# Kernel tuning notes

Hardware: AMD Instinct MI355X
Metric: run time of the kernel (lower is better)

The kernel has to match this reference:

```python
import jax, jax.numpy as jnp
import numpy as np

B, T = 64, 2048
D, H, L, OUT, V = 128, 256, 2, 64, 1000


def lstm_layer(x, Wih, Whh, bih, bhh):
    """Single-direction LSTM layer, PyTorch gate order (i, f, g, o).
    x: [B, T, Din] -> [B, T, H]"""
    Bn = x.shape[0]
    Hh = Whh.shape[1]
    # precompute input contribution to gates once: [B, T, 4H] -> time-major
    xg = jnp.einsum('btd,gd->btg', x, Wih) + bih
    xg = jnp.swapaxes(xg, 0, 1)  # [T, B, 4H]

    def step(carry, g_x):
        h, c = carry
        g = g_x + h @ Whh.T + bhh
        i, f, gg, o = jnp.split(g, 4, axis=-1)
        c = jax.nn.sigmoid(f) * c + jax.nn.sigmoid(i) * jnp.tanh(gg)
        h = jax.nn.sigmoid(o) * jnp.tanh(c)
        return (h, c), h

    h0 = jnp.zeros((Bn, Hh), x.dtype)
    (_, _), hs = jax.lax.scan(step, (h0, h0), xg)
    return jnp.swapaxes(hs, 0, 1)  # [B, T, H]


def setup_inputs() -> dict:
    key = jax.random.key(0)
    ks = jax.random.split(key, 12)
    s = 0.05
    inp = {
        'x': jax.random.randint(ks[0], (B, T), 0, V + 1, dtype=jnp.int32),
        'embed_table': jax.random.normal(ks[1], (V + 1, D), jnp.float32) * s,
        'W_ih0': jax.random.normal(ks[2], (4 * H, D), jnp.float32) * s,
        'W_hh0': jax.random.normal(ks[3], (4 * H, H), jnp.float32) * s,
        'b_ih0': jax.random.normal(ks[4], (4 * H,), jnp.float32) * s,
        'b_hh0': jax.random.normal(ks[5], (4 * H,), jnp.float32) * s,
        'W_ih1': jax.random.normal(ks[6], (4 * H, H), jnp.float32) * s,
        'W_hh1': jax.random.normal(ks[7], (4 * H, H), jnp.float32) * s,
        'b_ih1': jax.random.normal(ks[8], (4 * H,), jnp.float32) * s,
        'b_hh1': jax.random.normal(ks[9], (4 * H,), jnp.float32) * s,
        'fc_W': jax.random.normal(ks[10], (OUT, H), jnp.float32) * s,
        'fc_b': jax.random.normal(ks[11], (OUT,), jnp.float32) * s,
    }
    return inp


def reference(x, embed_table, W_ih0, W_hh0, b_ih0, b_hh0,
              W_ih1, W_hh1, b_ih1, b_hh1, fc_W, fc_b):
    # embedding + padding mask (padding_idx=0, masked_fill x==0 -> 0)
    e = embed_table[x]                              # [B, T, D]
    e = e * (x != 0)[..., None].astype(e.dtype)
    # 2-layer LSTM, zero initial state
    h = lstm_layer(e, W_ih0, W_hh0, b_ih0, b_hh0)   # [B, T, H]
    h = lstm_layer(h, W_ih1, W_hh1, b_ih1, b_hh1)   # [B, T, H]
    # linear + softmax over last dim
    logits = jnp.einsum('bth,oh->bto', h, fc_W) + fc_b
    return jax.nn.softmax(logits, axis=-1)
```

## Files before the change

kernel.cpp:

```cpp
#include <hip/hip_runtime.h>
#include <cstdint>
#include <cstddef>


typedef _Float16 half_t;
typedef _Float16 half8 __attribute__((ext_vector_type(8)));
typedef _Float16 half2t __attribute__((ext_vector_type(2)));
typedef float floatx4 __attribute__((ext_vector_type(4)));

#define B_   64
#define T_   2048
#define D_   128
#define H_   256
#define G4_  1024
#define OUT_ 64
#define MTOT (B_ * T_)

#define EVC  25
#define TLC  7
#define TL_BYTES (TLC * 1024 * 16)

#if defined(__has_builtin)
#if __has_builtin(__builtin_amdgcn_fdot2)
#define HAVE_FDOT2 1
#endif
#endif

__device__ __forceinline__ float dot2acc(unsigned w, unsigned h, float acc) {
  half2t a = __builtin_bit_cast(half2t, w);
  half2t b = __builtin_bit_cast(half2t, h);
#ifdef HAVE_FDOT2
  return __builtin_amdgcn_fdot2(a, b, acc, false);
#else
  return acc + (float)a[0] * (float)b[0] + (float)a[1] * (float)b[1];
#endif
}

__device__ __forceinline__ float fast_sigmoid(float x) {
  return 1.f / (1.f + __expf(-x));
}
__device__ __forceinline__ float fast_tanh(float x) {
  return 1.f - 2.f / (1.f + __expf(2.f * x));
}


__global__ __launch_bounds__(256) void k_cvt_f16(const float* __restrict__ in,
                                                 half_t* __restrict__ out, int n) {
  int i = blockIdx.x * 256 + threadIdx.x;
  if (i < n) out[i] = (half_t)in[i];
}

__global__ __launch_bounds__(256) void k_pack_whh(const float* __restrict__ whh,
                                                  half_t* __restrict__ wp) {
  int i = blockIdx.x * 256 + threadIdx.x;
  int e  = i & 7;
  int j  = (i >> 3) & 1023;
  int kc = i >> 13;
  wp[i] = (half_t)whh[j * 256 + kc * 8 + e];
}

__global__ __launch_bounds__(256) void k_bias(const float* __restrict__ a,
                                              const float* __restrict__ b,
                                              float* __restrict__ out, int n) {
  int i = blockIdx.x * 256 + threadIdx.x;
  if (i < n) out[i] = a[i] + b[i];
}

__global__ __launch_bounds__(256) void k_fcwt(const float* __restrict__ fcw,
                                              float* __restrict__ fcwt) {
  int i = blockIdx.x * 256 + threadIdx.x;
  fcwt[i] = fcw[(i & 63) * 256 + (i >> 6)];
}


__global__ __launch_bounds__(256) void k_embed(const int* __restrict__ x,
                                               const float* __restrict__ tab,
                                               half_t* __restrict__ e) {
  const long i = (long)blockIdx.x * 256 + threadIdx.x;
  const long m = i >> 4;
  const int ch = (int)(i & 15) * 8;
  const int xi = x[m];
  half8 v;
  #pragma unroll
  for (int q = 0; q < 8; ++q) v[q] = (half_t)0.f;
  if (xi != 0) {
    const float* p = tab + (long)xi * D_ + ch;
    #pragma unroll
    for (int q = 0; q < 8; ++q) v[q] = (half_t)p[q];
  }
  *(half8*)(e + m * D_ + ch) = v;
}


__global__ __launch_bounds__(256) void k_gemm_f16(const half_t* __restrict__ A,
                                                  const half_t* __restrict__ Wt,
                                                  const float* __restrict__ bias,
                                                  half_t* __restrict__ C,
                                                  int K, int N,
                                                  int rowShift, int strideB, int toff) {
  __shared__ half_t As[128][40];
  __shared__ half_t Bs[128][40];
  const int tid  = threadIdx.x;
  const int lane = tid & 63;
  const int wave = tid >> 6;
  const int wr = wave >> 1, wc = wave & 1;
  const int r0 = blockIdx.x * 128;
  const int n0 = blockIdx.y * 128;
  const int srow = tid >> 2;
  const int schunk = (tid & 3) * 8;
  const int rmask = (1 << rowShift) - 1;

  floatx4 zero = {0.f, 0.f, 0.f, 0.f};
  floatx4 acc[4][4];
  for (int i = 0; i < 4; ++i)
    for (int j = 0; j < 4; ++j) acc[i][j] = zero;

  const int ra = r0 + srow, rb = r0 + srow + 64;
  const half_t* ArowA = A + ((long)(ra >> rowShift) * strideB + toff + (ra & rmask)) * K;
  const half_t* ArowB = A + ((long)(rb >> rowShift) * strideB + toff + (rb & rmask)) * K;

  for (int k0 = 0; k0 < K; k0 += 32) {
    *(uint4*)(&As[srow][schunk])      = *(const uint4*)(ArowA + k0 + schunk);
    *(uint4*)(&As[srow + 64][schunk]) = *(const uint4*)(ArowB + k0 + schunk);
    const half_t* Bp = Wt + (long)(n0 + srow) * K + k0 + schunk;
    *(uint4*)(&Bs[srow][schunk])      = *(const uint4*)(Bp);
    *(uint4*)(&Bs[srow + 64][schunk]) = *(const uint4*)(Bp + 64L * K);
    __syncthreads();

    const int kq = (lane >> 4) * 8;
    const int fr = lane & 15;
    half8 af[4], bf[4];
    #pragma unroll
    for (int i = 0; i < 4; ++i) af[i] = *(const half8*)(&As[wr * 64 + i * 16 + fr][kq]);
    #pragma unroll
    for (int i = 0; i < 4; ++i) bf[i] = *(const half8*)(&Bs[wc * 64 + i * 16 + fr][kq]);
    #pragma unroll
    for (int mi = 0; mi < 4; ++mi)
      #pragma unroll
      for (int ni = 0; ni < 4; ++ni)
        acc[mi][ni] = __builtin_amdgcn_mfma_f32_16x16x32_f16(af[mi], bf[ni], acc[mi][ni], 0, 0, 0);
    __syncthreads();
  }

  const int fr = lane & 15, fq = lane >> 4;
  for (int ni = 0; ni < 4; ++ni) {
    const int gcol = n0 + wc * 64 + ni * 16 + fr;
    const float bv = bias[gcol];
    for (int mi = 0; mi < 4; ++mi) {
      const long grow = r0 + wr * 64 + mi * 16 + fq * 4;
      #pragma unroll
      for (int r = 0; r < 4; ++r)
        C[(grow + r) * (long)N + gcol] = (half_t)(acc[mi][ni][r] + bv);
    }
  }
}


__global__ __launch_bounds__(1024) void k_lstm_res(const half_t* __restrict__ xg,
                                                   const uint4* __restrict__ Wp,
                                                   half_t* __restrict__ hout,
                                                   float* __restrict__ c_state,
                                                   half_t* __restrict__ h_state,
                                                   int steps, int first) {
  extern __shared__ uint4 wtail[];
  __shared__ float gsh[1024];
  __shared__ __align__(16) half_t hsh[256];
  const int b = blockIdx.x;
  const int j = threadIdx.x;

  uint4 wv[EVC];
  #pragma unroll
  for (int kc = 0; kc < EVC; ++kc) wv[kc] = Wp[kc * 1024 + j];
  #pragma unroll
  for (int cc = 0; cc < TLC; ++cc) wtail[cc * 1024 + j] = Wp[(EVC + cc) * 1024 + j];

  float c = 0.f;
  if (j < H_) {
    if (first) {
      hsh[j] = (half_t)0.f;
    } else {
      hsh[j] = h_state[b * H_ + j];
      c = c_state[b * H_ + j];
    }
  }

  const half_t* xp = xg + (long)b * steps * G4_ + j;
  half_t* hp_out = hout + (long)b * steps * H_;
  half_t xv = xp[0];

  for (int t = 0; t < steps; ++t) {
    const int tn = (t + 1 < steps) ? t + 1 : t;
    half_t xnext = xp[(long)tn * G4_];
    __syncthreads();
    float acc = (float)xv;
    const uint4* hv4 = (const uint4*)hsh;
    #pragma unroll
    for (int kc = 0; kc < EVC; ++kc) {
      uint4 w = wv[kc];
      uint4 h4 = hv4[kc];
      acc = dot2acc(w.x, h4.x, acc);
      acc = dot2acc(w.y, h4.y, acc);
      acc = dot2acc(w.z, h4.z, acc);
      acc = dot2acc(w.w, h4.w, acc);
    }
    #pragma unroll
    for (int cc = 0; cc < TLC; ++cc) {
      uint4 w = wtail[cc * 1024 + j];
      uint4 h4 = hv4[EVC + cc];
      acc = dot2acc(w.x, h4.x, acc);
      acc = dot2acc(w.y, h4.y, acc);
      acc = dot2acc(w.z, h4.z, acc);
      acc = dot2acc(w.w, h4.w, acc);
    }
    gsh[j] = acc;
    xv = xnext;
    __syncthreads();
    if (j < H_) {
      float ig = fast_sigmoid(gsh[j]);
      float fg = fast_sigmoid(gsh[H_ + j]);
      float g2 = fast_tanh(gsh[2 * H_ + j]);
      float og = fast_sigmoid(gsh[3 * H_ + j]);
      c = fg * c + ig * g2;
      float h = og * fast_tanh(c);
      half_t hh = (half_t)h;
      hp_out[(long)t * H_ + j] = hh;
      hsh[j] = hh;
    }
  }
  if (j < H_) {
    c_state[b * H_ + j] = c;
    h_state[b * H_ + j] = hsh[j];
  }
}


__global__ __launch_bounds__(1024) void k_lstm(const half_t* __restrict__ xg,
                                               const uint4* __restrict__ Wp,
                                               half_t* __restrict__ hout,
                                               float* __restrict__ c_state,
                                               half_t* __restrict__ h_state,
                                               int steps, int first) {
  const int b = blockIdx.x;
  const int j = threadIdx.x;
  __shared__ float gsh[1024];
  __shared__ __align__(16) half_t hsh[256];
  float c = 0.f;
  if (j < H_) {
    if (first) {
      hsh[j] = (half_t)0.f;
    } else {
      hsh[j] = h_state[b * H_ + j];
      c = c_state[b * H_ + j];
    }
  }
  const uint4*  wp     = Wp + j;
  const half_t* xp     = xg + (long)b * steps * G4_ + j;
  half_t*       hp_out = hout + (long)b * steps * H_;
  for (int t = 0; t < steps; ++t) {
    __syncthreads();
    float acc = (float)xp[(long)t * G4_];
    const uint4* hv4 = (const uint4*)hsh;
    #pragma unroll 8
    for (int kc = 0; kc < 32; ++kc) {
      uint4 w  = wp[(long)kc * G4_];
      uint4 h4 = hv4[kc];
      acc = dot2acc(w.x, h4.x, acc);
      acc = dot2acc(w.y, h4.y, acc);
      acc = dot2acc(w.z, h4.z, acc);
      acc = dot2acc(w.w, h4.w, acc);
    }
    gsh[j] = acc;
    __syncthreads();
    if (j < H_) {
      float ig = fast_sigmoid(gsh[j]);
      float fg = fast_sigmoid(gsh[H_ + j]);
      float g2 = fast_tanh(gsh[2 * H_ + j]);
      float og = fast_sigmoid(gsh[3 * H_ + j]);
      c = fg * c + ig * g2;
      float h = og * fast_tanh(c);
      hp_out[(long)t * H_ + j] = (half_t)h;
      hsh[j] = (half_t)h;
    }
  }
  if (j < H_) {
    c_state[b * H_ + j] = c;
    h_state[b * H_ + j] = hsh[j];
  }
}


__global__ __launch_bounds__(256) void k_fc_softmax(const half_t* __restrict__ h2,
                                                    const float* __restrict__ fcwt,
                                                    const float* __restrict__ fcb,
                                                    float* __restrict__ out,
                                                    int rowShift, int strideB, int toff) {
  const int lane = threadIdx.x & 63;
  const int r = blockIdx.x * 4 + (threadIdx.x >> 6);
  const half_t* hr = h2 + (long)r * H_;
  float acc = fcb[lane];
  for (int kc = 0; kc < 32; ++kc) {
    uint4 hv = *(const uint4*)(hr + kc * 8);
    unsigned hu[4] = {hv.x, hv.y, hv.z, hv.w};
    #pragma unroll
    for (int p = 0; p < 4; ++p) {
      half2t hh = __builtin_bit_cast(half2t, hu[p]);
      acc += (float)hh[0] * fcwt[(kc * 8 + p * 2) * 64 + lane];
      acc += (float)hh[1] * fcwt[(kc * 8 + p * 2 + 1) * 64 + lane];
    }
  }
  float m = acc;
  #pragma unroll
  for (int off = 32; off > 0; off >>= 1) m = fmaxf(m, __shfl_xor(m, off));
  float e = __expf(acc - m);
  float s = e;
  #pragma unroll
  for (int off = 32; off > 0; off >>= 1) s += __shfl_xor(s, off);
  const long outrow = (long)(r >> rowShift) * strideB + toff + (r & ((1 << rowShift) - 1));
  out[outrow * OUT_ + lane] = e / s;
}


extern "C" void kernel_launch(void* const* d_in, const int* in_sizes, int n_in,
                              void* d_out, int out_size, void* d_ws, size_t ws_size,
                              hipStream_t stream) {
  const int*   x    = (const int*)d_in[0];
  const float* tab  = (const float*)d_in[1];
  const float* wih0 = (const float*)d_in[2];
  const float* whh0 = (const float*)d_in[3];
  const float* bih0 = (const float*)d_in[4];
  const float* bhh0 = (const float*)d_in[5];
  const float* wih1 = (const float*)d_in[6];
  const float* whh1 = (const float*)d_in[7];
  const float* bih1 = (const float*)d_in[8];
  const float* bhh1 = (const float*)d_in[9];
  const float* fcw  = (const float*)d_in[10];
  const float* fcb  = (const float*)d_in[11];

  char* p = (char*)d_ws;
  auto alloc = [&](size_t bytes) {
    void* r = (void*)p;
    p += (bytes + 255) & ~(size_t)255;
    return r;
  };
  half_t* wih0_h = (half_t*)alloc((size_t)G4_ * D_ * 2);
  half_t* wih1_h = (half_t*)alloc((size_t)G4_ * H_ * 2);
  half_t* wp0    = (half_t*)alloc((size_t)G4_ * H_ * 2);
  half_t* wp1    = (half_t*)alloc((size_t)G4_ * H_ * 2);
  float*  bias0  = (float*)alloc(G4_ * 4);
  float*  bias1  = (float*)alloc(G4_ * 4);
  float*  fcwt   = (float*)alloc((size_t)H_ * OUT_ * 4);
  half_t* hstate = (half_t*)alloc((size_t)2 * B_ * H_ * 2);
  float*  cstate = (float*)alloc((size_t)2 * B_ * H_ * 4);
  size_t fixed_used = (size_t)(p - (char*)d_ws);

  int CH = 2048;
  while (CH > 32 &&
         fixed_used + (size_t)CH * (131072 + 32768) + (1u << 20) > ws_size)
    CH >>= 1;
  const int rowShift = __builtin_ctz(CH);
  half_t* XG = (half_t*)alloc((size_t)CH * B_ * G4_ * 2);
  half_t* HB = (half_t*)alloc((size_t)CH * B_ * H_ * 2);
  half_t* ebuf = (half_t*)d_out;

  hipError_t attr_rc = hipFuncSetAttribute(
      reinterpret_cast<const void*>(k_lstm_res),
      hipFuncAttributeMaxDynamicSharedMemorySize, TL_BYTES);
  const bool use_res = (attr_rc == hipSuccess);

  k_cvt_f16<<<512, 256, 0, stream>>>(wih0, wih0_h, G4_ * D_);
  k_cvt_f16<<<1024, 256, 0, stream>>>(wih1, wih1_h, G4_ * H_);
  k_pack_whh<<<1024, 256, 0, stream>>>(whh0, wp0);
  k_pack_whh<<<1024, 256, 0, stream>>>(whh1, wp1);
  k_bias<<<4, 256, 0, stream>>>(bih0, bhh0, bias0, G4_);
  k_bias<<<4, 256, 0, stream>>>(bih1, bhh1, bias1, G4_);
  k_fcwt<<<64, 256, 0, stream>>>(fcw, fcwt);

  k_embed<<<MTOT * (D_ / 8) / 256, 256, 0, stream>>>(x, tab, ebuf);

  const int M = B_ * CH;
  const int nchunks = T_ / CH;
  for (int ci = 0; ci < nchunks; ++ci) {
    const int t0 = ci * CH;
    k_gemm_f16<<<dim3(M / 128, G4_ / 128), 256, 0, stream>>>(
        ebuf, wih0_h, bias0, XG, D_, G4_, rowShift, T_, t0);
    if (use_res)
      k_lstm_res<<<B_, 1024, TL_BYTES, stream>>>(XG, (const uint4*)wp0, HB,
                                                 cstate, hstate, CH, ci == 0);
    else
      k_lstm<<<B_, 1024, 0, stream>>>(XG, (const uint4*)wp0, HB,
                                      cstate, hstate, CH, ci == 0);
    k_gemm_f16<<<dim3(M / 128, G4_ / 128), 256, 0, stream>>>(
        HB, wih1_h, bias1, XG, H_, G4_, rowShift, CH, 0);
    if (use_res)
      k_lstm_res<<<B_, 1024, TL_BYTES, stream>>>(XG, (const uint4*)wp1, HB,
                                                 cstate + B_ * H_, hstate + B_ * H_,
                                                 CH, ci == 0);
    else
      k_lstm<<<B_, 1024, 0, stream>>>(XG, (const uint4*)wp1, HB,
                                      cstate + B_ * H_, hstate + B_ * H_,
                                      CH, ci == 0);
    k_fc_softmax<<<M / 4, 256, 0, stream>>>(HB, fcwt, fcb, (float*)d_out,
                                            rowShift, T_, t0);
  }
}
```

Baseline: 7.635 ms.

## Compute all four gates per thread in 256-thread LSTM blocks with double-buffered h

The recurrent LSTM kernel moves from 1024 threads (one gate row each) to 256 threads that each compute all four gate rows for one hidden unit. This removes the gate exchange through shared memory and one of the two barriers per timestep, since h is double-buffered. Each thread now holds 112 uint4 of weights in registers (448 VGPRs) with a small shared-memory tail, which relies on the large register file and risks spilling and lower latency hiding with only 4 waves per block.

New measurement: 18.05 ms. 136% more time.

```diff
diff --git a/kernel.cpp b/kernel.cpp
--- a/kernel.cpp
+++ b/kernel.cpp
@@ -16,9 +16,9 @@
 #define OUT_ 64
 #define MTOT (B_ * T_)
 
-#define EVC  25
-#define TLC  7
-#define TL_BYTES (TLC * 1024 * 16)
+#define EVC2 28
+#define TLC2 4
+#define TL2_BYTES (TLC2 * 4 * 256 * 16)
 
 #if defined(__has_builtin)
 #if __has_builtin(__builtin_amdgcn_fdot2)
@@ -57,6 +57,16 @@
   int j  = (i >> 3) & 1023;
   int kc = i >> 13;
   wp[i] = (half_t)whh[j * 256 + kc * 8 + e];
+}
+
+__global__ __launch_bounds__(256) void k_pack_whh_q(const float* __restrict__ whh,
+                                                    half_t* __restrict__ wq) {
+  int i = blockIdx.x * 256 + threadIdx.x;
+  int e  = i & 7;
+  int j  = (i >> 3) & 255;
+  int kc = (i >> 11) & 31;
+  int rr = (i >> 16) & 3;
+  wq[i] = (half_t)whh[(rr * 256 + j) * 256 + kc * 8 + e];
 }
 
 __global__ __launch_bounds__(256) void k_bias(const float* __restrict__ a,
@@ -156,81 +166,90 @@
 }
 
 
-__global__ __launch_bounds__(1024) void k_lstm_res(const half_t* __restrict__ xg,
-                                                   const uint4* __restrict__ Wp,
-                                                   half_t* __restrict__ hout,
-                                                   float* __restrict__ c_state,
-                                                   half_t* __restrict__ h_state,
-                                                   int steps, int first) {
+__global__ __launch_bounds__(256, 1) void k_lstm_res2(const half_t* __restrict__ xg,
+                                                      const uint4* __restrict__ Wq,
+                                                      half_t* __restrict__ hout,
+                                                      float* __restrict__ c_state,
+                                                      half_t* __restrict__ h_state,
+                                                      int steps, int first) {
   extern __shared__ uint4 wtail[];
-  __shared__ float gsh[1024];
-  __shared__ __align__(16) half_t hsh[256];
+  __shared__ __align__(16) half_t hsh[2][256];
   const int b = blockIdx.x;
   const int j = threadIdx.x;
 
-  uint4 wv[EVC];
+  uint4 wv[4 * EVC2];
   #pragma unroll
-  for (int kc = 0; kc < EVC; ++kc) wv[kc] = Wp[kc * 1024 + j];
+  for (int rr = 0; rr < 4; ++rr)
+    #pragma unroll
+    for (int kc = 0; kc < EVC2; ++kc)
+      wv[rr * EVC2 + kc] = Wq[(rr * 32 + kc) * 256 + j];
   #pragma unroll
-  for (int cc = 0; cc < TLC; ++cc) wtail[cc * 1024 + j] = Wp[(EVC + cc) * 1024 + j];
+  for (int rr = 0; rr < 4; ++rr)
+    #pragma unroll
+    for (int cc = 0; cc < TLC2; ++cc)
+      wtail[(cc * 4 + rr) * 256 + j] = Wq[(rr * 32 + EVC2 + cc) * 256 + j];
 
   float c = 0.f;
-  if (j < H_) {
-    if (first) {
-      hsh[j] = (half_t)0.f;
-    } else {
-      hsh[j] = h_state[b * H_ + j];
-      c = c_state[b * H_ + j];
-    }
-  }
+  if (first) {
+    hsh[0][j] = (half_t)0.f;
+  } else {
+    hsh[0][j] = h_state[b * H_ + j];
+    c = c_state[b * H_ + j];
+  }
+  __syncthreads();
 
   const half_t* xp = xg + (long)b * steps * G4_ + j;
-  half_t* hp_out = hout + (long)b * steps * H_;
-  half_t xv = xp[0];
+  half_t* hp_out = hout + (long)b * steps * H_ + j;
+  half_t hlast = hsh[0][j];
 
   for (int t = 0; t < steps; ++t) {
-    const int tn = (t + 1 < steps) ? t + 1 : t;
-    half_t xnext = xp[(long)tn * G4_];
+    const half_t* xr = xp + (long)t * G4_;
+    float x0 = (float)xr[0];
+    float x1 = (float)xr[256];
+    float x2 = (float)xr[512];
+    float x3 = (float)xr[768];
+
+    const uint4* hb = (const uint4*)hsh[t & 1];
+    float a0 = 0.f, a1 = 0.f, a2 = 0.f, a3 = 0.f;
+    #pragma unroll
+    for (int kc = 0; kc < 32; ++kc) {
+      uint4 h4 = hb[kc];
+      uint4 w0, w1, w2, w3;
+      if (kc < EVC2) {
+        w0 = wv[0 * EVC2 + kc];
+        w1 = wv[1 * EVC2 + kc];
+        w2 = wv[2 * EVC2 + kc];
+        w3 = wv[3 * EVC2 + kc];
+      } else {
+        w0 = wtail[((kc - EVC2) * 4 + 0) * 256 + j];
+        w1 = wtail[((kc - EVC2) * 4 + 1) * 256 + j];
+        w2 = wtail[((kc - EVC2) * 4 + 2) * 256 + j];
+        w3 = wtail[((kc - EVC2) * 4 + 3) * 256 + j];
+      }
+      a0 = dot2acc(w0.x, h4.x, a0); a0 = dot2acc(w0.y, h4.y, a0);
+      a0 = dot2acc(w0.z, h4.z, a0); a0 = dot2acc(w0.w, h4.w, a0);
+      a1 = dot2acc(w1.x, h4.x, a1); a1 = dot2acc(w1.y, h4.y, a1);
+      a1 = dot2acc(w1.z, h4.z, a1); a1 = dot2acc(w1.w, h4.w, a1);
+      a2 = dot2acc(w2.x, h4.x, a2); a2 = dot2acc(w2.y, h4.y, a2);
+      a2 = dot2acc(w2.z, h4.z, a2); a2 = dot2acc(w2.w, h4.w, a2);
+      a3 = dot2acc(w3.x, h4.x, a3); a3 = dot2acc(w3.y, h4.y, a3);
+      a3 = dot2acc(w3.z, h4.z, a3); a3 = dot2acc(w3.w, h4.w, a3);
+    }
+
+    float ig = fast_sigmoid(a0 + x0);
+    float fg = fast_sigmoid(a1 + x1);
+    float g2 = fast_tanh(a2 + x2);
+    float og = fast_sigmoid(a3 + x3);
+    c = fg * c + ig * g2;
+    float h = og * fast_tanh(c);
+    half_t hh = (half_t)h;
+    hp_out[(long)t * H_] = hh;
+    hsh[(t + 1) & 1][j] = hh;
+    hlast = hh;
     __syncthreads();
-    float acc = (float)xv;
-    const uint4* hv4 = (const uint4*)hsh;
-    #pragma unroll
-    for (int kc = 0; kc < EVC; ++kc) {
-      uint4 w = wv[kc];
-      uint4 h4 = hv4[kc];
-      acc = dot2acc(w.x, h4.x, acc);
-      acc = dot2acc(w.y, h4.y, acc);
-      acc = dot2acc(w.z, h4.z, acc);
-      acc = dot2acc(w.w, h4.w, acc);
-    }
-    #pragma unroll
-    for (int cc = 0; cc < TLC; ++cc) {
-      uint4 w = wtail[cc * 1024 + j];
-      uint4 h4 = hv4[EVC + cc];
-      acc = dot2acc(w.x, h4.x, acc);
-      acc = dot2acc(w.y, h4.y, acc);
-      acc = dot2acc(w.z, h4.z, acc);
-      acc = dot2acc(w.w, h4.w, acc);
-    }
-    gsh[j] = acc;
-    xv = xnext;
-    __syncthreads();
-    if (j < H_) {
-      float ig = fast_sigmoid(gsh[j]);
-      float fg = fast_sigmoid(gsh[H_ + j]);
-      float g2 = fast_tanh(gsh[2 * H_ + j]);
-      float og = fast_sigmoid(gsh[3 * H_ + j]);
-      c = fg * c + ig * g2;
-      float h = og * fast_tanh(c);
-      half_t hh = (half_t)h;
-      hp_out[(long)t * H_ + j] = hh;
-      hsh[j] = hh;
-    }
-  }
-  if (j < H_) {
-    c_state[b * H_ + j] = c;
-    h_state[b * H_ + j] = hsh[j];
-  }
+  }
+  c_state[b * H_ + j] = c;
+  h_state[b * H_ + j] = hlast;
 }
 
 
@@ -344,6 +363,8 @@
   };
   half_t* wih0_h = (half_t*)alloc((size_t)G4_ * D_ * 2);
   half_t* wih1_h = (half_t*)alloc((size_t)G4_ * H_ * 2);
+  half_t* wq0    = (half_t*)alloc((size_t)G4_ * H_ * 2);
+  half_t* wq1    = (half_t*)alloc((size_t)G4_ * H_ * 2);
   half_t* wp0    = (half_t*)alloc((size_t)G4_ * H_ * 2);
   half_t* wp1    = (half_t*)alloc((size_t)G4_ * H_ * 2);
   float*  bias0  = (float*)alloc(G4_ * 4);
@@ -363,12 +384,14 @@
   half_t* ebuf = (half_t*)d_out;
 
   hipError_t attr_rc = hipFuncSetAttribute(
-      reinterpret_cast<const void*>(k_lstm_res),
-      hipFuncAttributeMaxDynamicSharedMemorySize, TL_BYTES);
+      reinterpret_cast<const void*>(k_lstm_res2),
+      hipFuncAttributeMaxDynamicSharedMemorySize, TL2_BYTES);
   const bool use_res = (attr_rc == hipSuccess);
 
   k_cvt_f16<<<512, 256, 0, stream>>>(wih0, wih0_h, G4_ * D_);
   k_cvt_f16<<<1024, 256, 0, stream>>>(wih1, wih1_h, G4_ * H_);
+  k_pack_whh_q<<<1024, 256, 0, stream>>>(whh0, wq0);
+  k_pack_whh_q<<<1024, 256, 0, stream>>>(whh1, wq1);
   k_pack_whh<<<1024, 256, 0, stream>>>(whh0, wp0);
   k_pack_whh<<<1024, 256, 0, stream>>>(whh1, wp1);
   k_bias<<<4, 256, 0, stream>>>(bih0, bhh0, bias0, G4_);
@@ -384,17 +407,17 @@
     k_gemm_f16<<<dim3(M / 128, G4_ / 128), 256, 0, stream>>>(
         ebuf, wih0_h, bias0, XG, D_, G4_, rowShift, T_, t0);
     if (use_res)
-      k_lstm_res<<<B_, 1024, TL_BYTES, stream>>>(XG, (const uint4*)wp0, HB,
-                                                 cstate, hstate, CH, ci == 0);
+      k_lstm_res2<<<B_, 256, TL2_BYTES, stream>>>(XG, (const uint4*)wq0, HB,
+                                                  cstate, hstate, CH, ci == 0);
     else
       k_lstm<<<B_, 1024, 0, stream>>>(XG, (const uint4*)wp0, HB,
                                       cstate, hstate, CH, ci == 0);
     k_gemm_f16<<<dim3(M / 128, G4_ / 128), 256, 0, stream>>>(
         HB, wih1_h, bias1, XG, H_, G4_, rowShift, CH, 0);
     if (use_res)
-      k_lstm_res<<<B_, 1024, TL_BYTES, stream>>>(XG, (const uint4*)wp1, HB,
-                                                 cstate + B_ * H_, hstate + B_ * H_,
-                                                 CH, ci == 0);
+      k_lstm_res2<<<B_, 256, TL2_BYTES, stream>>>(XG, (const uint4*)wq1, HB,
+                                                  cstate + B_ * H_, hstate + B_ * H_,
+                                                  CH, ci == 0);
     else
       k_lstm<<<B_, 1024, 0, stream>>>(XG, (const uint4*)wp1, HB,
                                       cstate + B_ * H_, hstate + B_ * H_,
```

## Rewrite recurrent LSTM step as per-batch MFMA matvec with register-resident weights

Applied to the files above, without the earlier changes.

Replaces the 1024-thread fdot2 recurrent kernel with a 256-thread kernel. Each wave computes 256 gate rows via 16x16x32 f16 MFMA, with weights pre-packed into MFMA fragment layout: 104 fragments per lane stay in registers and 24 go to LDS. The hidden state is double-buffered in shared memory, and the x-gate contribution is added after the matvec. The aim is fewer threads and faster recurrent matvecs per timestep. In exchange it wastes 15/16 of the MFMA columns (batch 1 per block) and puts heavy pressure on registers.

Measured after the change: 11.92 ms. +56.1%, slower.

```diff
diff --git a/kernel.cpp b/kernel.cpp
--- a/kernel.cpp
+++ b/kernel.cpp
@@ -16,9 +16,9 @@
 #define OUT_ 64
 #define MTOT (B_ * T_)
 
-#define EVC  25
-#define TLC  7
-#define TL_BYTES (TLC * 1024 * 16)
+#define RFRAGS 104
+#define LFRAGS 24
+#define LDSW_BYTES (4 * LFRAGS * 64 * 16)
 
 #if defined(__has_builtin)
 #if __has_builtin(__builtin_amdgcn_fdot2)
@@ -57,6 +57,19 @@
   int j  = (i >> 3) & 1023;
   int kc = i >> 13;
   wp[i] = (half_t)whh[j * 256 + kc * 8 + e];
+}
+
+__global__ __launch_bounds__(256) void k_pack_whh_frag(const float* __restrict__ whh,
+                                                       half_t* __restrict__ wqf) {
+  int i = blockIdx.x * 256 + threadIdx.x;
+  int e  = i & 7;
+  int l  = (i >> 3) & 63;
+  int kc = (i >> 9) & 7;
+  int rt = (i >> 12) & 15;
+  int w  = (i >> 16) & 3;
+  int row = w * 256 + rt * 16 + (l & 15);
+  int col = kc * 32 + (l >> 4) * 8 + e;
+  wqf[i] = (half_t)whh[row * 256 + col];
 }
 
 __global__ __launch_bounds__(256) void k_bias(const float* __restrict__ a,
@@ -156,81 +169,94 @@
 }
 
 
-__global__ __launch_bounds__(1024) void k_lstm_res(const half_t* __restrict__ xg,
-                                                   const uint4* __restrict__ Wp,
-                                                   half_t* __restrict__ hout,
-                                                   float* __restrict__ c_state,
-                                                   half_t* __restrict__ h_state,
-                                                   int steps, int first) {
-  extern __shared__ uint4 wtail[];
-  __shared__ float gsh[1024];
-  __shared__ __align__(16) half_t hsh[256];
+__global__ __launch_bounds__(256, 1) void k_lstm_v3(const half_t* __restrict__ xg,
+                                                    const uint4* __restrict__ wqf,
+                                                    half_t* __restrict__ hout,
+                                                    float* __restrict__ c_state,
+                                                    half_t* __restrict__ h_state,
+                                                    int steps, int first) {
+  extern __shared__ uint4 wlds[];
+  __shared__ __align__(16) half_t hsh[2][256];
+  __shared__ __align__(16) float gsh[1024];
   const int b = blockIdx.x;
-  const int j = threadIdx.x;
-
-  uint4 wv[EVC];
+  const int tid = threadIdx.x;
+  const int w = tid >> 6, l = tid & 63;
+  const int j = tid;
+
+  half8 wv[RFRAGS];
+  const uint4* wbase = wqf + (size_t)w * 128 * 64;
   #pragma unroll
-  for (int kc = 0; kc < EVC; ++kc) wv[kc] = Wp[kc * 1024 + j];
+  for (int i = 0; i < RFRAGS; ++i)
+    wv[i] = __builtin_bit_cast(half8, wbase[i * 64 + l]);
   #pragma unroll
-  for (int cc = 0; cc < TLC; ++cc) wtail[cc * 1024 + j] = Wp[(EVC + cc) * 1024 + j];
+  for (int i = 0; i < LFRAGS; ++i)
+    wlds[(w * LFRAGS + i) * 64 + l] = wbase[(RFRAGS + i) * 64 + l];
 
   float c = 0.f;
-  if (j < H_) {
-    if (first) {
-      hsh[j] = (half_t)0.f;
-    } else {
-      hsh[j] = h_state[b * H_ + j];
-      c = c_state[b * H_ + j];
-    }
-  }
-
-  const half_t* xp = xg + (long)b * steps * G4_ + j;
-  half_t* hp_out = hout + (long)b * steps * H_;
-  half_t xv = xp[0];
+  if (first) {
+    hsh[0][j] = (half_t)0.f;
+  } else {
+    hsh[0][j] = h_state[b * H_ + j];
+    c = c_state[b * H_ + j];
+  }
+  __syncthreads();
+
+  const half_t* xgb = xg + (long)b * steps * G4_;
+  half_t* hp_out = hout + (long)b * steps * H_ + j;
 
   for (int t = 0; t < steps; ++t) {
-    const int tn = (t + 1 < steps) ? t + 1 : t;
-    half_t xnext = xp[(long)tn * G4_];
-    __syncthreads();
-    float acc = (float)xv;
-    const uint4* hv4 = (const uint4*)hsh;
-    #pragma unroll
-    for (int kc = 0; kc < EVC; ++kc) {
-      uint4 w = wv[kc];
-      uint4 h4 = hv4[kc];
-      acc = dot2acc(w.x, h4.x, acc);
-      acc = dot2acc(w.y, h4.y, acc);
-      acc = dot2acc(w.z, h4.z, acc);
-      acc = dot2acc(w.w, h4.w, acc);
-    }
-    #pragma unroll
-    for (int cc = 0; cc < TLC; ++cc) {
-      uint4 w = wtail[cc * 1024 + j];
-      uint4 h4 = hv4[EVC + cc];
-      acc = dot2acc(w.x, h4.x, acc);
-      acc = dot2acc(w.y, h4.y, acc);
-      acc = dot2acc(w.z, h4.z, acc);
-      acc = dot2acc(w.w, h4.w, acc);
-    }
-    gsh[j] = acc;
-    xv = xnext;
-    __syncthreads();
-    if (j < H_) {
-      float ig = fast_sigmoid(gsh[j]);
-      float fg = fast_sigmoid(gsh[H_ + j]);
-      float g2 = fast_tanh(gsh[2 * H_ + j]);
-      float og = fast_sigmoid(gsh[3 * H_ + j]);
-      c = fg * c + ig * g2;
-      float h = og * fast_tanh(c);
-      half_t hh = (half_t)h;
-      hp_out[(long)t * H_ + j] = hh;
-      hsh[j] = hh;
-    }
-  }
-  if (j < H_) {
-    c_state[b * H_ + j] = c;
-    h_state[b * H_ + j] = hsh[j];
-  }
+    const half_t* xr = xgb + (long)t * G4_;
+    float x0 = (float)xr[j];
+    float x1 = (float)xr[256 + j];
+    float x2 = (float)xr[512 + j];
+    float x3 = (float)xr[768 + j];
+
+    const half_t* hp = hsh[t & 1];
+    half8 bf[8];
+    #pragma unroll
+    for (int kc = 0; kc < 8; ++kc)
+      bf[kc] = *(const half8*)(hp + kc * 32 + ((l >> 4) << 3));
+
+    #pragma unroll
+    for (int rt = 0; rt < 13; ++rt) {
+      floatx4 acc = {0.f, 0.f, 0.f, 0.f};
+      #pragma unroll
+      for (int kc = 0; kc < 8; ++kc)
+        acc = __builtin_amdgcn_mfma_f32_16x16x32_f16(wv[rt * 8 + kc], bf[kc], acc, 0, 0, 0);
+      if ((l & 15) == 0)
+        *(floatx4*)&gsh[w * 256 + rt * 16 + ((l >> 4) << 2)] = acc;
+    }
+    #pragma unroll
+    for (int rt = 13; rt < 16; ++rt) {
+      floatx4 acc = {0.f, 0.f, 0.f, 0.f};
+      #pragma unroll
+      for (int kc = 0; kc < 8; ++kc) {
+        half8 wf = __builtin_bit_cast(half8,
+            wlds[(w * LFRAGS + (rt - 13) * 8 + kc) * 64 + l]);
+        acc = __builtin_amdgcn_mfma_f32_16x16x32_f16(wf, bf[kc], acc, 0, 0, 0);
+      }
+      if ((l & 15) == 0)
+        *(floatx4*)&gsh[w * 256 + rt * 16 + ((l >> 4) << 2)] = acc;
+    }
+    __syncthreads();
+
+    float gi = gsh[j]       + x0;
+    float gf = gsh[256 + j] + x1;
+    float gg = gsh[512 + j] + x2;
+    float go = gsh[768 + j] + x3;
+    float ig = fast_sigmoid(gi);
+    float fg = fast_sigmoid(gf);
+    float g2 = fast_tanh(gg);
+    float og = fast_sigmoid(go);
+    c = fg * c + ig * g2;
+    float h = og * fast_tanh(c);
+    half_t hh = (half_t)h;
+    hp_out[(long)t * H_] = hh;
+    hsh[(t + 1) & 1][j] = hh;
+    __syncthreads();
+  }
+  c_state[b * H_ + j] = c;
+  h_state[b * H_ + j] = (half_t)hsh[steps & 1][j];
 }
 
 
@@ -344,6 +370,8 @@
   };
   half_t* wih0_h = (half_t*)alloc((size_t)G4_ * D_ * 2);
   half_t* wih1_h = (half_t*)alloc((size_t)G4_ * H_ * 2);
+  half_t* wqf0   = (half_t*)alloc((size_t)G4_ * H_ * 2);
+  half_t* wqf1   = (half_t*)alloc((size_t)G4_ * H_ * 2);
   half_t* wp0    = (half_t*)alloc((size_t)G4_ * H_ * 2);
   half_t* wp1    = (half_t*)alloc((size_t)G4_ * H_ * 2);
   float*  bias0  = (float*)alloc(G4_ * 4);
@@ -363,12 +391,14 @@
   half_t* ebuf = (half_t*)d_out;
 
   hipError_t attr_rc = hipFuncSetAttribute(
-      reinterpret_cast<const void*>(k_lstm_res),
-      hipFuncAttributeMaxDynamicSharedMemorySize, TL_BYTES);
+      reinterpret_cast<const void*>(k_lstm_v3),
+      hipFuncAttributeMaxDynamicSharedMemorySize, LDSW_BYTES);
   const bool use_res = (attr_rc == hipSuccess);
 
   k_cvt_f16<<<512, 256, 0, stream>>>(wih0, wih0_h, G4_ * D_);
   k_cvt_f16<<<1024, 256, 0, stream>>>(wih1, wih1_h, G4_ * H_);
+  k_pack_whh_frag<<<1024, 256, 0, stream>>>(whh0, wqf0);
+  k_pack_whh_frag<<<1024, 256, 0, stream>>>(whh1, wqf1);
   k_pack_whh<<<1024, 256, 0, stream>>>(whh0, wp0);
   k_pack_whh<<<1024, 256, 0, stream>>>(whh1, wp1);
   k_bias<<<4, 256, 0, stream>>>(bih0, bhh0, bias0, G4_);
@@ -384,7 +414,7 @@
     k_gemm_f16<<<dim3(M / 128, G4_ / 128), 256, 0, stream>>>(
         ebuf, wih0_h, bias0, XG, D_, G4_, rowShift, T_, t0);
     if (use_res)
-      k_lstm_res<<<B_, 1024, TL_BYTES, stream>>>(XG, (const uint4*)wp0, HB,
+      k_lstm_v3<<<B_, 256, LDSW_BYTES, stream>>>(XG, (const uint4*)wqf0, HB,
                                                  cstate, hstate, CH, ci == 0);
     else
       k_lstm<<<B_, 1024, 0, stream>>>(XG, (const uint4*)wp0, HB,
@@ -392,7 +422,7 @@
     k_gemm_f16<<<dim3(M / 128, G4_ / 128), 256, 0, stream>>>(
         HB, wih1_h, bias1, XG, H_, G4_, rowShift, CH, 0);
     if (use_res)
-      k_lstm_res<<<B_, 1024, TL_BYTES, stream>>>(XG, (const uint4*)wp1, HB,
+      k_lstm_v3<<<B_, 256, LDSW_BYTES, stream>>>(XG, (const uint4*)wqf1, HB,
                                                  cstate + B_ * H_, hstate + B_ * H_,
                                                  CH, ci == 0);
     else
```
